# Performance work log

Hardware: AMD Instinct MI355X
Metric: run time of the kernel (lower is better)

## Reference

```python
import jax, jax.numpy as jnp
import numpy as np

NUM_HEADS = 16


def _local_attn(q, k, v, bias, nq, nk):
    """Blocked local attention, faithful to rearrange_to_dense_trunk semantics.
    q,k,v: [B,H,N,D]; bias: [B,Hb,N,N] (Hb broadcasts against H).
    Trunk i (queries [i*nq,(i+1)*nq)) attends keys at original indices
    [i*nq - pad_left, i*nq - pad_left + nk); out-of-range keys/values/bias are
    zero-padded (the module pads with zeros, no -inf key masking).
    Assumes N % nq == 0 (q_pad_length == 0, so the query mask loop is a no-op).
    """
    B, H, N, D = q.shape
    T = N // nq                      # n_trunks
    pad_left = (nk - nq) // 2
    Lp = (T - 1) * nq + nk           # padded key length so every window is full
    pad_right = Lp - pad_left - N
    k_p = jnp.pad(k, ((0, 0), (0, 0), (pad_left, pad_right), (0, 0)))
    v_p = jnp.pad(v, ((0, 0), (0, 0), (pad_left, pad_right), (0, 0)))
    b_p = jnp.pad(bias, ((0, 0), (0, 0), (0, 0), (pad_left, pad_right)))
    # window gather indices: [T, nk]
    kidx = jnp.arange(T)[:, None] * nq + jnp.arange(nk)[None, :]
    k_t = k_p[:, :, kidx, :]         # [B,H,T,nk,D]
    v_t = v_p[:, :, kidx, :]         # [B,H,T,nk,D]
    Bb, Hb = bias.shape[0], bias.shape[1]
    b_r = b_p.reshape(Bb, Hb, T, nq, Lp)
    b_t = jnp.take_along_axis(b_r, kidx[None, None, :, None, :], axis=-1)  # [Bb,Hb,T,nq,nk]
    q_t = q.reshape(B, H, T, nq, D)
    scores = jnp.einsum('bhtqd,bhtkd->bhtqk', q_t, k_t) + b_t
    w = jax.nn.softmax(scores, axis=-1)
    o = jnp.einsum('bhtqk,bhtkd->bhtqd', w, v_t)
    return o.reshape(B, H, N, D)


def setup_inputs() -> dict:
    key = jax.random.key(0)
    ks = jax.random.split(key, 8)
    B, N, C = 1, 4096, 256
    H, D = NUM_HEADS, 64
    HD = H * D
    q_x = jax.random.normal(ks[0], (B, N, C), dtype=jnp.float32)
    kv_x = jax.random.normal(ks[1], (B, N, C), dtype=jnp.float32)
    attn_bias = jax.random.normal(ks[2], (B, 1, N, N), dtype=jnp.float32) * 0.1
    Wq = jax.random.normal(ks[3], (C, HD), dtype=jnp.float32) / np.sqrt(C).astype(np.float32)
    Wk = jax.random.normal(ks[4], (C, HD), dtype=jnp.float32) / np.sqrt(C).astype(np.float32)
    Wv = jax.random.normal(ks[5], (C, HD), dtype=jnp.float32) / np.sqrt(C).astype(np.float32)
    Wg = jax.random.normal(ks[6], (C, HD), dtype=jnp.float32) / np.sqrt(C).astype(np.float32)
    Wo = jax.random.normal(ks[7], (HD, C), dtype=jnp.float32) / np.sqrt(HD).astype(np.float32)
    return {"q_x": q_x, "kv_x": kv_x, "attn_bias": attn_bias,
            "Wq": Wq, "Wk": Wk, "Wv": Wv, "Wg": Wg, "Wo": Wo,
            "n_queries": 64, "n_keys": 256}


def reference(q_x, kv_x, attn_bias, Wq, Wk, Wv, Wg, Wo, n_queries, n_keys):
    B, N, C = q_x.shape
    H = NUM_HEADS
    D = Wq.shape[-1] // H
    def split_heads(x):
        return x.reshape(B, N, H, D).transpose(0, 2, 1, 3)  # [B,H,N,D]
    q = split_heads(q_x @ Wq) / jnp.sqrt(jnp.float32(D))
    k = split_heads(kv_x @ Wk)
    v = split_heads(kv_x @ Wv)
    o = _local_attn(q, k, v, attn_bias, n_queries, n_keys)
    o = o.transpose(0, 2, 1, 3).reshape(B, N, H * D)
    g = jax.nn.sigmoid(q_x @ Wg)  # gating head
    return (o * g) @ Wo
```

## Files before the change

kernel.cpp:

```cpp
#include <hip/hip_runtime.h>

#define N_ 4096
#define C_ 256
#define H_ 16
#define D_ 64
#define HD_ 1024

typedef __attribute__((ext_vector_type(8))) _Float16 f16x8;
typedef __attribute__((ext_vector_type(4))) _Float16 f16x4;
typedef __attribute__((ext_vector_type(4))) float f32x4;

__device__ __forceinline__ void gload16(const void* g, void* l) {
    __builtin_amdgcn_global_load_lds(
        (const __attribute__((address_space(1))) unsigned int*)g,
        (__attribute__((address_space(3))) unsigned int*)l, 16, 0, 0);
}

__global__ __launch_bounds__(256) void convert_kernel(
    const float* __restrict__ q_x, const float* __restrict__ kv_x,
    const float* __restrict__ Wq, const float* __restrict__ Wk,
    const float* __restrict__ Wv, const float* __restrict__ Wg,
    const float* __restrict__ Wo,
    _Float16* __restrict__ Xf, _Float16* __restrict__ WTf,
    _Float16* __restrict__ WoTf)
{
    __shared__ float ts[64][65];
    const int b = blockIdx.x;
    const int tid = threadIdx.x;

    if (b < 512) {
        const int seg = b >> 8;
        const float* src = seg ? kv_x : q_x;
        _Float16* df = Xf + (size_t)seg * 1048576;
        const int base = (b & 255) * 4096 + tid * 16;
#pragma unroll
        for (int q = 0; q < 4; ++q) {
            float4 v = *(const float4*)&src[base + q * 4];
            f16x4 fv;
            fv[0] = (_Float16)v.x; fv[1] = (_Float16)v.y;
            fv[2] = (_Float16)v.z; fv[3] = (_Float16)v.w;
            *(f16x4*)&df[base + q * 4] = fv;
        }
        return;
    }

    const float* src;
    _Float16* df;
    int srcC, dstC, r0, c0;
    if (b < 768) {
        const int widx = (b - 512) >> 6;
        const int tile = (b - 512) & 63;
        src = (widx == 0) ? Wq : (widx == 1) ? Wk : (widx == 2) ? Wv : Wg;
        df = WTf + (size_t)widx * 262144;
        srcC = 1024; dstC = 256;
        r0 = (tile >> 4) * 64;
        c0 = (tile & 15) * 64;
    } else {
        const int tile = b - 768;
        src = Wo; df = WoTf;
        srcC = 256; dstC = 1024;
        r0 = (tile >> 2) * 64;
        c0 = (tile & 3) * 64;
    }
    {
        const int r = tid >> 2;
        const int cch = (tid & 3) * 16;
#pragma unroll
        for (int q = 0; q < 4; ++q) {
            float4 v = *(const float4*)&src[(size_t)(r0 + r) * srcC + c0 + cch + q * 4];
            ts[r][cch + q * 4 + 0] = v.x;
            ts[r][cch + q * 4 + 1] = v.y;
            ts[r][cch + q * 4 + 2] = v.z;
            ts[r][cch + q * 4 + 3] = v.w;
        }
    }
    __syncthreads();
    {
        const int c = tid >> 2;
        const int rch = (tid & 3) * 16;
#pragma unroll
        for (int q = 0; q < 4; ++q) {
            f16x4 fv;
#pragma unroll
            for (int j = 0; j < 4; ++j)
                fv[j] = (_Float16)ts[rch + q * 4 + j][c];
            *(f16x4*)&df[(size_t)(c0 + c) * dstC + r0 + rch + q * 4] = fv;
        }
    }
}

__global__ __launch_bounds__(256) void proj_mfma(
    const _Float16* __restrict__ Xf, const _Float16* __restrict__ WTf,
    _Float16* __restrict__ qh, _Float16* __restrict__ kh,
    _Float16* __restrict__ vt, _Float16* __restrict__ gh)
{
    __shared__ __align__(16) char psmem[24576];
    _Float16* As = (_Float16*)psmem;
    _Float16* Bs = (_Float16*)(psmem + 8192);

    const int lb  = blockIdx.x;
    const int xcd = lb & 7;
    const int gr  = (lb >> 6) * 8 + xcd;
    const int g   = gr >> 6;
    const int m0  = (gr & 63) * 64;
    const int c0  = ((lb >> 3) & 7) * 128;

    const _Float16* A = Xf + ((g == 1 || g == 2) ? 1048576 : 0);
    const _Float16* B = WTf + (size_t)g * 262144;

    const int tid  = threadIdx.x;
    const int wv   = tid >> 6;
    const int lane = tid & 63;
    const int frow = lane & 15;
    const int grp  = lane >> 4;

    f32x4 acc[8];
#pragma unroll
    for (int j = 0; j < 8; ++j) acc[j] = (f32x4){0.f, 0.f, 0.f, 0.f};

    const int srow = tid >> 3;
    const int sch  = tid & 7;

    for (int kt = 0; kt < 256; kt += 64) {
        __syncthreads();
#pragma unroll
        for (int p = 0; p < 2; ++p) {
            const int row = p * 32 + srow;
            const int koff = kt + ((sch ^ (row & 7)) << 3);
            gload16(A + (size_t)(m0 + row) * 256 + koff, (char*)As + p * 4096 + tid * 16);
        }
#pragma unroll
        for (int p = 0; p < 4; ++p) {
            const int row = p * 32 + srow;
            const int koff = kt + ((sch ^ (row & 7)) << 3);
            gload16(B + (size_t)(c0 + row) * 256 + koff, (char*)Bs + p * 4096 + tid * 16);
        }
        __syncthreads();

#pragma unroll
        for (int ks = 0; ks < 2; ++ks) {
            const int ra = wv * 16 + frow;
            const f16x8 af = *(const f16x8*)((char*)As + ra * 128 + (((ks * 4 + grp) ^ (ra & 7)) << 4));
#pragma unroll
            for (int j = 0; j < 8; ++j) {
                const int rb = j * 16 + frow;
                const f16x8 bf = *(const f16x8*)((char*)Bs + rb * 128 + (((ks * 4 + grp) ^ (rb & 7)) << 4));
                acc[j] = __builtin_amdgcn_mfma_f32_16x16x32_f16(af, bf, acc[j], 0, 0, 0);
            }
        }
    }

    if (g == 2) {
#pragma unroll
        for (int j = 0; j < 8; ++j) {
            const int dglob = c0 + j * 16 + frow;
            const int n = m0 + wv * 16 + grp * 4;
            f16x4 pv;
#pragma unroll
            for (int v = 0; v < 4; ++v) pv[v] = (_Float16)acc[j][v];
            *(f16x4*)&vt[((size_t)dglob << 12) + n] = pv;
        }
        return;
    }

    __syncthreads();
    _Float16* Epi = (_Float16*)psmem;
    {
        const float scale = (g == 0) ? 0.125f : 1.f;
#pragma unroll
        for (int j = 0; j < 8; ++j) {
            const int rr = wv * 16 + grp * 4;
            const int cc = j * 16 + frow;
#pragma unroll
            for (int v = 0; v < 4; ++v) {
                float x = acc[j][v];
                x = (g == 3) ? 1.f / (1.f + __expf(-x)) : x * scale;
                Epi[(rr + v) * 136 + cc] = (_Float16)x;
            }
        }
    }
    __syncthreads();
    {
        const int ch   = tid & 15;
        const int head = ch >> 3;
        const int e8   = (ch & 7) * 8;
#pragma unroll
        for (int p = 0; p < 4; ++p) {
            const int r = p * 16 + (tid >> 4);
            const f16x8 val = *(const f16x8*)&Epi[r * 136 + head * 64 + e8];
            const int n = m0 + r;
            if (g == 3) {
                *(f16x8*)&gh[(size_t)n * HD_ + c0 + head * 64 + e8] = val;
            } else {
                _Float16* dst = (g == 0) ? qh : kh;
                const int hh = (c0 >> 6) + head;
                *(f16x8*)&dst[((size_t)hh * N_ + n) * D_ + e8] = val;
            }
        }
    }
}

__global__ __launch_bounds__(256, 4) void attn_mfma(
    const _Float16* __restrict__ qh, const _Float16* __restrict__ kh,
    const _Float16* __restrict__ vt, const float* __restrict__ bias,
    const _Float16* __restrict__ gh, _Float16* __restrict__ of)
{
    __shared__ __align__(16) char smem[40960];
    _Float16* Qs = (_Float16*)smem;
    char* Ks = smem + 8192;
    char* Ps = smem;
    char* Vs = smem + 16384;
    float* Oe = (float*)smem;

    const int lb  = blockIdx.x;
    const int xcd = lb & 7;
    const int j_  = lb >> 3;
    const int h   = j_ >> 3;
    const int t   = xcd * 8 + (j_ & 7);
    const int tid = threadIdx.x;
    const int lane = tid & 63;
    const int wv = tid >> 6;
    const int frow = lane & 15;
    const int grp = lane >> 4;
    const int kbase = t * 64 - 96;

    const char* qbase = (const char*)qh + (size_t)(h * N_ + t * 64) * 128;
    const char* kbase_p = (const char*)kh + (size_t)h * N_ * 128;

#pragma unroll
    for (int q = 0; q < 2; ++q) {
        const int lin = q * 4096 + tid * 16;
        const int row = lin >> 7;
        const int ch = (lin >> 4) & 7;
        gload16(qbase + row * 128 + ((ch ^ (row & 7)) << 4), (char*)Qs + lin);
    }
#pragma unroll
    for (int q = 0; q < 8; ++q) {
        const int lin = q * 4096 + tid * 16;
        const int row = lin >> 7;
        const int ch = (lin >> 4) & 7;
        const int kg = kbase + row;
        if ((unsigned)kg < (unsigned)N_) {
            gload16(kbase_p + (size_t)kg * 128 + ((ch ^ (row & 7)) << 4), Ks + lin);
        } else {
            *(float4*)(Ks + lin) = make_float4(0.f, 0.f, 0.f, 0.f);
        }
    }

    f32x4 sacc[16];
    {
        const int rowg = t * 64 + wv * 16 + grp * 4;
#pragma unroll
        for (int j = 0; j < 16; ++j) {
            const int colg = kbase + j * 16 + frow;
            const bool ok = (unsigned)colg < (unsigned)N_;
#pragma unroll
            for (int v = 0; v < 4; ++v)
                sacc[j][v] = ok ? bias[(size_t)(rowg + v) * N_ + colg] : 0.f;
        }
    }
    __syncthreads();

    {
        const int rq = wv * 16 + frow;
#pragma unroll
        for (int ks = 0; ks < 2; ++ks) {
            const f16x8 aq = *(const f16x8*)((char*)Qs + rq * 128 + (((ks * 4 + grp) ^ (rq & 7)) << 4));
#pragma unroll
            for (int j = 0; j < 16; ++j) {
                const int rk = j * 16 + frow;
                const f16x8 bk = *(const f16x8*)(Ks + rk * 128 + (((ks * 4 + grp) ^ (rk & 7)) << 4));
                sacc[j] = __builtin_amdgcn_mfma_f32_16x16x32_f16(aq, bk, sacc[j], 0, 0, 0);
            }
        }
    }
    __syncthreads();

    float inv[4];
    f32x4 oacc[4];
#pragma unroll
    for (int jd = 0; jd < 4; ++jd) oacc[jd] = (f32x4){0.f, 0.f, 0.f, 0.f};

#pragma unroll
    for (int c = 0; c < 2; ++c) {
        const int cb = kbase + c * 128;
        const bool bnd = (c == 0) ? (t <= 1) : (t >= 62);
        {
#pragma unroll
            for (int q = 0; q < 4; ++q) {
                const int lin = q * 4096 + tid * 16;
                const int d  = lin >> 8;
                const int cs = (lin >> 4) & 15;
                const int cl = (cs & 8) | ((cs & 7) ^ (d & 7));
                const int kg0 = cb + cl * 8;
                const int kgc = kg0 < 0 ? 0 : (kg0 > N_ - 8 ? N_ - 8 : kg0);
                gload16(vt + (((size_t)(h * 64 + d)) << 12) + kgc, Vs + lin);
            }
        }
        if (c == 0) {
#pragma unroll
            for (int v = 0; v < 4; ++v) {
                float m = sacc[0][v];
#pragma unroll
                for (int f = 1; f < 16; ++f) m = fmaxf(m, sacc[f][v]);
                m = fmaxf(m, __shfl_xor(m, 1));
                m = fmaxf(m, __shfl_xor(m, 2));
                m = fmaxf(m, __shfl_xor(m, 4));
                m = fmaxf(m, __shfl_xor(m, 8));
                float l = 0.f;
#pragma unroll
                for (int f = 0; f < 16; ++f) {
                    float e = __expf(sacc[f][v] - m);
                    sacc[f][v] = e;
                    l += e;
                }
                l += __shfl_xor(l, 1);
                l += __shfl_xor(l, 2);
                l += __shfl_xor(l, 4);
                l += __shfl_xor(l, 8);
                inv[v] = 1.f / l;
            }
        }
        {
#pragma unroll
            for (int j = 0; j < 8; ++j) {
#pragma unroll
                for (int v = 0; v < 4; ++v) {
                    const int r = wv * 16 + grp * 4 + v;
                    const int byt = r * 256 + ((j * 32 + frow * 2) ^ ((r & 7) << 4));
                    *(_Float16*)(Ps + byt) = (_Float16)sacc[c * 8 + j][v];
                }
            }
        }
        __syncthreads();
        if (bnd) {
#pragma unroll
            for (int q = 0; q < 4; ++q) {
                const int lin = q * 4096 + tid * 16;
                const int d  = lin >> 8;
                const int cs = (lin >> 4) & 15;
                const int cl = (cs & 8) | ((cs & 7) ^ (d & 7));
                const int kg0 = cb + cl * 8;
                if ((unsigned)kg0 >= (unsigned)N_)
                    *(float4*)(Vs + lin) = make_float4(0.f, 0.f, 0.f, 0.f);
            }
            __syncthreads();
        }
        const int rp = wv * 16 + frow;
#pragma unroll
        for (int ks = 0; ks < 4; ++ks) {
            const f16x8 ap = *(const f16x8*)(Ps + rp * 256 + (((ks * 4 + grp) ^ (rp & 7)) << 4));
#pragma unroll
            for (int jd = 0; jd < 4; ++jd) {
                const int rd = jd * 16 + frow;
                const f16x8 bv = *(const f16x8*)(Vs + rd * 256 + (((ks * 4 + grp) ^ (rd & 7)) << 4));
                oacc[jd] = __builtin_amdgcn_mfma_f32_16x16x32_f16(ap, bv, oacc[jd], 0, 0, 0);
            }
        }
        __syncthreads();
    }

#pragma unroll
    for (int jd = 0; jd < 4; ++jd) {
        const int dcol = jd * 16 + frow;
#pragma unroll
        for (int v = 0; v < 4; ++v) {
            const int rn = wv * 16 + grp * 4 + v;
            Oe[rn * 68 + dcol] = oacc[jd][v] * inv[v];
        }
    }
    __syncthreads();
    {
        const int r   = tid >> 2;
        const int seg = tid & 3;
        const int n   = t * 64 + r;
        const int cg0 = h * 64 + seg * 16;
        const float* orow = &Oe[r * 68 + seg * 16];
        f32x4 o0 = *(const f32x4*)&orow[0];
        f32x4 o1 = *(const f32x4*)&orow[4];
        f32x4 o2 = *(const f32x4*)&orow[8];
        f32x4 o3 = *(const f32x4*)&orow[12];
        const f16x8 g0 = *(const f16x8*)&gh[(size_t)n * HD_ + cg0];
        const f16x8 g1 = *(const f16x8*)&gh[(size_t)n * HD_ + cg0 + 8];
        f16x8 r0, r1;
#pragma unroll
        for (int e = 0; e < 4; ++e) {
            r0[e]     = (_Float16)(o0[e] * (float)g0[e]);
            r0[4 + e] = (_Float16)(o1[e] * (float)g0[4 + e]);
            r1[e]     = (_Float16)(o2[e] * (float)g1[e]);
            r1[4 + e] = (_Float16)(o3[e] * (float)g1[4 + e]);
        }
        *(f16x8*)&of[(size_t)n * HD_ + cg0]     = r0;
        *(f16x8*)&of[(size_t)n * HD_ + cg0 + 8] = r1;
    }
}

__global__ __launch_bounds__(256) void out_mfma(
    const _Float16* __restrict__ of, const _Float16* __restrict__ WoTf,
    float* __restrict__ out)
{
    __shared__ __align__(16) char smem[24576];

    const int lb  = blockIdx.x;
    const int xcd = lb & 7;
    const int s   = lb >> 3;
    const int rowt = (s >> 2) * 8 + xcd;
    const int m0  = rowt * 32;
    const int c0  = (s & 3) * 64;

    const int tid  = threadIdx.x;
    const int wave = tid >> 6;
    const int lane = tid & 63;
    const int wr   = wave >> 1;
    const int wc   = wave & 1;
    const int frow = lane & 15;
    const int grp  = lane >> 4;

    f32x4 acc[2];
#pragma unroll
    for (int j = 0; j < 2; ++j) acc[j] = (f32x4){0.f, 0.f, 0.f, 0.f};

    auto STAGE = [&](char* bb, int kt) {
        {
            const int row = tid >> 3;
            const int ch  = tid & 7;
            const int koff = kt + ((ch ^ (row & 7)) << 3);
            gload16(of + (size_t)(m0 + row) * HD_ + koff, bb + tid * 16);
        }
#pragma unroll
        for (int p = 0; p < 2; ++p) {
            const int lin = p * 4096 + tid * 16;
            const int row = lin >> 7;
            const int ch  = (lin >> 4) & 7;
            const int koff = kt + ((ch ^ (row & 7)) << 3);
            gload16(WoTf + (size_t)(c0 + row) * HD_ + koff, bb + 4096 + lin);
        }
    };

    STAGE(smem, 0);
    __syncthreads();

    for (int t = 0; t < 16; ++t) {
        char* cur = smem + (t & 1) * 12288;
        if (t < 15) STAGE(smem + ((t + 1) & 1) * 12288, (t + 1) * 64);

        _Float16* As = (_Float16*)cur;
        _Float16* Bs = (_Float16*)(cur + 4096);
#pragma unroll
        for (int ks = 0; ks < 2; ++ks) {
            const int ra = wr * 16 + frow;
            const f16x8 af = *(const f16x8*)((char*)As + ra * 128 + (((ks * 4 + grp) ^ (ra & 7)) << 4));
#pragma unroll
            for (int j = 0; j < 2; ++j) {
                const int rb = wc * 32 + j * 16 + frow;
                const f16x8 bf = *(const f16x8*)((char*)Bs + rb * 128 + (((ks * 4 + grp) ^ (rb & 7)) << 4));
                acc[j] = __builtin_amdgcn_mfma_f32_16x16x32_f16(af, bf, acc[j], 0, 0, 0);
            }
        }
        __syncthreads();
    }

    const int rbase = grp * 4;
#pragma unroll
    for (int j = 0; j < 2; ++j) {
        const int c = c0 + wc * 32 + j * 16 + frow;
#pragma unroll
        for (int v = 0; v < 4; ++v) {
            const int n = m0 + wr * 16 + rbase + v;
            out[(size_t)n * C_ + c] = acc[j][v];
        }
    }
}

extern "C" void kernel_launch(void* const* d_in, const int* in_sizes, int n_in,
                              void* d_out, int out_size, void* d_ws, size_t ws_size,
                              hipStream_t stream)
{
    const float* q_x  = (const float*)d_in[0];
    const float* kv_x = (const float*)d_in[1];
    const float* bias = (const float*)d_in[2];
    const float* Wq   = (const float*)d_in[3];
    const float* Wk   = (const float*)d_in[4];
    const float* Wv   = (const float*)d_in[5];
    const float* Wg   = (const float*)d_in[6];
    const float* Wo   = (const float*)d_in[7];
    float* out = (float*)d_out;

    char* ws = (char*)d_ws;
    const size_t MB = 1048576;
    _Float16* qh   = (_Float16*)(ws);
    _Float16* kh   = (_Float16*)(ws + 8  * MB);
    _Float16* vt   = (_Float16*)(ws + 16 * MB);
    _Float16* gh   = (_Float16*)(ws + 24 * MB);
    _Float16* of   = (_Float16*)(ws + 32 * MB);
    _Float16* Xf   = (_Float16*)(ws + 40 * MB);
    _Float16* WTf  = (_Float16*)(ws + 44 * MB);
    _Float16* WoTf = (_Float16*)(ws + 46 * MB);

    convert_kernel<<<832, 256, 0, stream>>>(q_x, kv_x, Wq, Wk, Wv, Wg, Wo,
                                            Xf, WTf, WoTf);
    proj_mfma<<<2048, 256, 0, stream>>>(Xf, WTf, qh, kh, vt, gh);
    attn_mfma<<<1024, 256, 0, stream>>>(qh, kh, vt, bias, gh, of);
    out_mfma<<<512, 256, 0, stream>>>(of, WoTf, out);
}
```

Before: 161.5 us.

## Pre-pack bias windows transposed for vector loads; shrink out-projection tiles

```diff
diff --git a/kernel.cpp b/kernel.cpp
--- a/kernel.cpp
+++ b/kernel.cpp
@@ -18,11 +18,12 @@
 
 __global__ __launch_bounds__(256) void convert_kernel(
     const float* __restrict__ q_x, const float* __restrict__ kv_x,
+    const float* __restrict__ bias,
     const float* __restrict__ Wq, const float* __restrict__ Wk,
     const float* __restrict__ Wv, const float* __restrict__ Wg,
     const float* __restrict__ Wo,
     _Float16* __restrict__ Xf, _Float16* __restrict__ WTf,
-    _Float16* __restrict__ WoTf)
+    _Float16* __restrict__ WoTf, float* __restrict__ bpF)
 {
     __shared__ float ts[64][65];
     const int b = blockIdx.x;
@@ -40,6 +41,45 @@
             fv[0] = (_Float16)v.x; fv[1] = (_Float16)v.y;
             fv[2] = (_Float16)v.z; fv[3] = (_Float16)v.w;
             *(f16x4*)&df[base + q * 4] = fv;
+        }
+        return;
+    }
+
+    if (b >= 832) {
+        const int t = b - 832;
+        const int kb = t * 64 - 96;
+        float* bpT = bpF + (size_t)t * 16384;
+#pragma unroll
+        for (int cc = 0; cc < 4; ++cc) {
+            if (cc) __syncthreads();
+            {
+                const int q = tid >> 2;
+                const float* brow = bias + (size_t)(t * 64 + q) * 4096;
+#pragma unroll
+                for (int u = 0; u < 4; ++u) {
+                    const int lc = (tid & 3) * 16 + u * 4;
+                    const int kg = kb + cc * 64 + lc;
+                    float4 v = make_float4(0.f, 0.f, 0.f, 0.f);
+                    if ((unsigned)kg < 4093u) v = *(const float4*)&brow[kg];
+                    ts[q][lc + 0] = v.x; ts[q][lc + 1] = v.y;
+                    ts[q][lc + 2] = v.z; ts[q][lc + 3] = v.w;
+                }
+            }
+            __syncthreads();
+            {
+                const int s = tid >> 2;
+                const int qseg = (tid & 3) * 16;
+                float* drow = bpT + (size_t)(cc * 64 + s) * 64 + qseg;
+#pragma unroll
+                for (int u = 0; u < 4; ++u) {
+                    float4 v;
+                    v.x = ts[qseg + u * 4 + 0][s];
+                    v.y = ts[qseg + u * 4 + 1][s];
+                    v.z = ts[qseg + u * 4 + 2][s];
+                    v.w = ts[qseg + u * 4 + 3][s];
+                    *(float4*)&drow[u * 4] = v;
+                }
+            }
         }
         return;
     }
@@ -202,7 +242,7 @@
 
 __global__ __launch_bounds__(256, 4) void attn_mfma(
     const _Float16* __restrict__ qh, const _Float16* __restrict__ kh,
-    const _Float16* __restrict__ vt, const float* __restrict__ bias,
+    const _Float16* __restrict__ vt, const float* __restrict__ bpF,
     const _Float16* __restrict__ gh, _Float16* __restrict__ of)
 {
     __shared__ __align__(16) char smem[40960];
@@ -249,15 +289,11 @@
 
     f32x4 sacc[16];
     {
-        const int rowg = t * 64 + wv * 16 + grp * 4;
-#pragma unroll
-        for (int j = 0; j < 16; ++j) {
-            const int colg = kbase + j * 16 + frow;
-            const bool ok = (unsigned)colg < (unsigned)N_;
-#pragma unroll
-            for (int v = 0; v < 4; ++v)
-                sacc[j][v] = ok ? bias[(size_t)(rowg + v) * N_ + colg] : 0.f;
-        }
+        const float* bpT = bpF + (size_t)t * 16384;
+        const int q0 = wv * 16 + grp * 4;
+#pragma unroll
+        for (int j = 0; j < 16; ++j)
+            sacc[j] = *(const f32x4*)&bpT[(j * 16 + frow) * 64 + q0];
     }
     __syncthreads();
 
@@ -399,14 +435,14 @@
     const _Float16* __restrict__ of, const _Float16* __restrict__ WoTf,
     float* __restrict__ out)
 {
-    __shared__ __align__(16) char smem[24576];
+    __shared__ __align__(16) char smem[16384];
 
     const int lb  = blockIdx.x;
     const int xcd = lb & 7;
     const int s   = lb >> 3;
-    const int rowt = (s >> 2) * 8 + xcd;
+    const int rowt = (s >> 3) * 8 + xcd;
     const int m0  = rowt * 32;
-    const int c0  = (s & 3) * 64;
+    const int c0  = (s & 7) * 32;
 
     const int tid  = threadIdx.x;
     const int wave = tid >> 6;
@@ -416,33 +452,22 @@
     const int frow = lane & 15;
     const int grp  = lane >> 4;
 
-    f32x4 acc[2];
-#pragma unroll
-    for (int j = 0; j < 2; ++j) acc[j] = (f32x4){0.f, 0.f, 0.f, 0.f};
+    f32x4 acc = (f32x4){0.f, 0.f, 0.f, 0.f};
 
     auto STAGE = [&](char* bb, int kt) {
-        {
-            const int row = tid >> 3;
-            const int ch  = tid & 7;
-            const int koff = kt + ((ch ^ (row & 7)) << 3);
-            gload16(of + (size_t)(m0 + row) * HD_ + koff, bb + tid * 16);
-        }
-#pragma unroll
-        for (int p = 0; p < 2; ++p) {
-            const int lin = p * 4096 + tid * 16;
-            const int row = lin >> 7;
-            const int ch  = (lin >> 4) & 7;
-            const int koff = kt + ((ch ^ (row & 7)) << 3);
-            gload16(WoTf + (size_t)(c0 + row) * HD_ + koff, bb + 4096 + lin);
-        }
+        const int row = tid >> 3;
+        const int ch  = tid & 7;
+        const int koff = kt + ((ch ^ (row & 7)) << 3);
+        gload16(of + (size_t)(m0 + row) * HD_ + koff, bb + tid * 16);
+        gload16(WoTf + (size_t)(c0 + row) * HD_ + koff, bb + 4096 + tid * 16);
     };
 
     STAGE(smem, 0);
     __syncthreads();
 
     for (int t = 0; t < 16; ++t) {
-        char* cur = smem + (t & 1) * 12288;
-        if (t < 15) STAGE(smem + ((t + 1) & 1) * 12288, (t + 1) * 64);
+        char* cur = smem + (t & 1) * 8192;
+        if (t < 15) STAGE(smem + ((t + 1) & 1) * 8192, (t + 1) * 64);
 
         _Float16* As = (_Float16*)cur;
         _Float16* Bs = (_Float16*)(cur + 4096);
@@ -450,24 +475,20 @@
         for (int ks = 0; ks < 2; ++ks) {
             const int ra = wr * 16 + frow;
             const f16x8 af = *(const f16x8*)((char*)As + ra * 128 + (((ks * 4 + grp) ^ (ra & 7)) << 4));
-#pragma unroll
-            for (int j = 0; j < 2; ++j) {
-                const int rb = wc * 32 + j * 16 + frow;
-                const f16x8 bf = *(const f16x8*)((char*)Bs + rb * 128 + (((ks * 4 + grp) ^ (rb & 7)) << 4));
-                acc[j] = __builtin_amdgcn_mfma_f32_16x16x32_f16(af, bf, acc[j], 0, 0, 0);
-            }
+            const int rb = wc * 16 + frow;
+            const f16x8 bf = *(const f16x8*)((char*)Bs + rb * 128 + (((ks * 4 + grp) ^ (rb & 7)) << 4));
+            acc = __builtin_amdgcn_mfma_f32_16x16x32_f16(af, bf, acc, 0, 0, 0);
         }
         __syncthreads();
     }
 
-    const int rbase = grp * 4;
-#pragma unroll
-    for (int j = 0; j < 2; ++j) {
-        const int c = c0 + wc * 32 + j * 16 + frow;
+    {
+        const int c = c0 + wc * 16 + frow;
+        const int rbase = grp * 4;
 #pragma unroll
         for (int v = 0; v < 4; ++v) {
             const int n = m0 + wr * 16 + rbase + v;
-            out[(size_t)n * C_ + c] = acc[j][v];
+            out[(size_t)n * C_ + c] = acc[v];
         }
     }
 }
@@ -496,10 +517,11 @@
     _Float16* Xf   = (_Float16*)(ws + 40 * MB);
     _Float16* WTf  = (_Float16*)(ws + 44 * MB);
     _Float16* WoTf = (_Float16*)(ws + 46 * MB);
-
-    convert_kernel<<<832, 256, 0, stream>>>(q_x, kv_x, Wq, Wk, Wv, Wg, Wo,
-                                            Xf, WTf, WoTf);
+    float*    bpF  = (float*)   (ws + 48 * MB);
+
+    convert_kernel<<<896, 256, 0, stream>>>(q_x, kv_x, bias, Wq, Wk, Wv, Wg, Wo,
+                                            Xf, WTf, WoTf, bpF);
     proj_mfma<<<2048, 256, 0, stream>>>(Xf, WTf, qh, kh, vt, gh);
-    attn_mfma<<<1024, 256, 0, stream>>>(qh, kh, vt, bias, gh, of);
-    out_mfma<<<512, 256, 0, stream>>>(of, WoTf, out);
+    attn_mfma<<<1024, 256, 0, stream>>>(qh, kh, vt, bpF, gh, of);
+    out_mfma<<<1024, 256, 0, stream>>>(of, WoTf, out);
 }
```

New measurement: 161.6 us. No clear change (+0.0%).

## Fuse all four stages into one persistent cooperative kernel with grid syncs

Applied to the files above, without the earlier changes.

```diff
diff --git a/kernel.cpp b/kernel.cpp
--- a/kernel.cpp
+++ b/kernel.cpp
@@ -1,4 +1,7 @@
 #include <hip/hip_runtime.h>
+#include <hip/hip_cooperative_groups.h>
+
+namespace cg = cooperative_groups;
 
 #define N_ 4096
 #define C_ 256
@@ -14,6 +17,462 @@
     __builtin_amdgcn_global_load_lds(
         (const __attribute__((address_space(1))) unsigned int*)g,
         (__attribute__((address_space(3))) unsigned int*)l, 16, 0, 0);
+}
+
+__device__ __forceinline__ void phase_sync(cg::grid_group& g) {
+    __threadfence();
+    g.sync();
+    __threadfence();
+}
+
+__global__ __launch_bounds__(256) void fused_all(
+    const float* __restrict__ q_x, const float* __restrict__ kv_x,
+    const float* __restrict__ bias,
+    const float* __restrict__ Wq, const float* __restrict__ Wk,
+    const float* __restrict__ Wv, const float* __restrict__ Wg,
+    const float* __restrict__ Wo,
+    _Float16* __restrict__ Xf, _Float16* __restrict__ WTf,
+    _Float16* __restrict__ WoTf,
+    _Float16* __restrict__ qh, _Float16* __restrict__ kh,
+    _Float16* __restrict__ vt, _Float16* __restrict__ gh,
+    _Float16* __restrict__ of, float* __restrict__ out)
+{
+    __shared__ __align__(16) char smem[40960];
+    cg::grid_group grid = cg::this_grid();
+    const int nb  = gridDim.x;
+    const int bid = blockIdx.x;
+    const int tid = threadIdx.x;
+
+    for (int b = bid; b < 832; b += nb) {
+        float (*ts)[65] = (float(*)[65])smem;
+        if (b < 512) {
+            const int seg = b >> 8;
+            const float* src = seg ? kv_x : q_x;
+            _Float16* df = Xf + (size_t)seg * 1048576;
+            const int base = (b & 255) * 4096 + tid * 16;
+#pragma unroll
+            for (int q = 0; q < 4; ++q) {
+                float4 v = *(const float4*)&src[base + q * 4];
+                f16x4 fv;
+                fv[0] = (_Float16)v.x; fv[1] = (_Float16)v.y;
+                fv[2] = (_Float16)v.z; fv[3] = (_Float16)v.w;
+                *(f16x4*)&df[base + q * 4] = fv;
+            }
+        } else {
+            const float* src;
+            _Float16* df;
+            int srcC, dstC, r0, c0;
+            if (b < 768) {
+                const int widx = (b - 512) >> 6;
+                const int tile = (b - 512) & 63;
+                src = (widx == 0) ? Wq : (widx == 1) ? Wk : (widx == 2) ? Wv : Wg;
+                df = WTf + (size_t)widx * 262144;
+                srcC = 1024; dstC = 256;
+                r0 = (tile >> 4) * 64;
+                c0 = (tile & 15) * 64;
+            } else {
+                const int tile = b - 768;
+                src = Wo; df = WoTf;
+                srcC = 256; dstC = 1024;
+                r0 = (tile >> 2) * 64;
+                c0 = (tile & 3) * 64;
+            }
+            {
+                const int r = tid >> 2;
+                const int cch = (tid & 3) * 16;
+#pragma unroll
+                for (int q = 0; q < 4; ++q) {
+                    float4 v = *(const float4*)&src[(size_t)(r0 + r) * srcC + c0 + cch + q * 4];
+                    ts[r][cch + q * 4 + 0] = v.x;
+                    ts[r][cch + q * 4 + 1] = v.y;
+                    ts[r][cch + q * 4 + 2] = v.z;
+                    ts[r][cch + q * 4 + 3] = v.w;
+                }
+            }
+            __syncthreads();
+            {
+                const int c = tid >> 2;
+                const int rch = (tid & 3) * 16;
+#pragma unroll
+                for (int q = 0; q < 4; ++q) {
+                    f16x4 fv;
+#pragma unroll
+                    for (int j = 0; j < 4; ++j)
+                        fv[j] = (_Float16)ts[rch + q * 4 + j][c];
+                    *(f16x4*)&df[(size_t)(c0 + c) * dstC + r0 + rch + q * 4] = fv;
+                }
+            }
+            __syncthreads();
+        }
+    }
+    phase_sync(grid);
+
+    for (int lb = bid; lb < 2048; lb += nb) {
+        _Float16* As = (_Float16*)smem;
+        _Float16* Bs = (_Float16*)(smem + 8192);
+
+        const int xcd = lb & 7;
+        const int gr  = (lb >> 6) * 8 + xcd;
+        const int g   = gr >> 6;
+        const int m0  = (gr & 63) * 64;
+        const int c0  = ((lb >> 3) & 7) * 128;
+
+        const _Float16* A = Xf + ((g == 1 || g == 2) ? 1048576 : 0);
+        const _Float16* B = WTf + (size_t)g * 262144;
+
+        const int wv   = tid >> 6;
+        const int lane = tid & 63;
+        const int frow = lane & 15;
+        const int grp  = lane >> 4;
+
+        f32x4 acc[8];
+#pragma unroll
+        for (int j = 0; j < 8; ++j) acc[j] = (f32x4){0.f, 0.f, 0.f, 0.f};
+
+        const int srow = tid >> 3;
+        const int sch  = tid & 7;
+
+        for (int kt = 0; kt < 256; kt += 64) {
+            __syncthreads();
+#pragma unroll
+            for (int p = 0; p < 2; ++p) {
+                const int row = p * 32 + srow;
+                const int koff = kt + ((sch ^ (row & 7)) << 3);
+                gload16(A + (size_t)(m0 + row) * 256 + koff, (char*)As + p * 4096 + tid * 16);
+            }
+#pragma unroll
+            for (int p = 0; p < 4; ++p) {
+                const int row = p * 32 + srow;
+                const int koff = kt + ((sch ^ (row & 7)) << 3);
+                gload16(B + (size_t)(c0 + row) * 256 + koff, (char*)Bs + p * 4096 + tid * 16);
+            }
+            __syncthreads();
+
+#pragma unroll
+            for (int ks = 0; ks < 2; ++ks) {
+                const int ra = wv * 16 + frow;
+                const f16x8 af = *(const f16x8*)((char*)As + ra * 128 + (((ks * 4 + grp) ^ (ra & 7)) << 4));
+#pragma unroll
+                for (int j = 0; j < 8; ++j) {
+                    const int rb = j * 16 + frow;
+                    const f16x8 bf = *(const f16x8*)((char*)Bs + rb * 128 + (((ks * 4 + grp) ^ (rb & 7)) << 4));
+                    acc[j] = __builtin_amdgcn_mfma_f32_16x16x32_f16(af, bf, acc[j], 0, 0, 0);
+                }
+            }
+        }
+
+        if (g == 2) {
+#pragma unroll
+            for (int j = 0; j < 8; ++j) {
+                const int dglob = c0 + j * 16 + frow;
+                const int n = m0 + wv * 16 + grp * 4;
+                f16x4 pv;
+#pragma unroll
+                for (int v = 0; v < 4; ++v) pv[v] = (_Float16)acc[j][v];
+                *(f16x4*)&vt[((size_t)dglob << 12) + n] = pv;
+            }
+            __syncthreads();
+        } else {
+            __syncthreads();
+            _Float16* Epi = (_Float16*)smem;
+            {
+                const float scale = (g == 0) ? 0.125f : 1.f;
+#pragma unroll
+                for (int j = 0; j < 8; ++j) {
+                    const int rr = wv * 16 + grp * 4;
+                    const int cc = j * 16 + frow;
+#pragma unroll
+                    for (int v = 0; v < 4; ++v) {
+                        float x = acc[j][v];
+                        x = (g == 3) ? 1.f / (1.f + __expf(-x)) : x * scale;
+                        Epi[(rr + v) * 136 + cc] = (_Float16)x;
+                    }
+                }
+            }
+            __syncthreads();
+            {
+                const int ch   = tid & 15;
+                const int head = ch >> 3;
+                const int e8   = (ch & 7) * 8;
+#pragma unroll
+                for (int p = 0; p < 4; ++p) {
+                    const int r = p * 16 + (tid >> 4);
+                    const f16x8 val = *(const f16x8*)&Epi[r * 136 + head * 64 + e8];
+                    const int n = m0 + r;
+                    if (g == 3) {
+                        *(f16x8*)&gh[(size_t)n * HD_ + c0 + head * 64 + e8] = val;
+                    } else {
+                        _Float16* dst = (g == 0) ? qh : kh;
+                        const int hh = (c0 >> 6) + head;
+                        *(f16x8*)&dst[((size_t)hh * N_ + n) * D_ + e8] = val;
+                    }
+                }
+            }
+            __syncthreads();
+        }
+    }
+    phase_sync(grid);
+
+    for (int ab = bid; ab < 1024; ab += nb) {
+        _Float16* Qs = (_Float16*)smem;
+        char* Ks = smem + 8192;
+        char* Ps = smem;
+        char* Vs = smem + 16384;
+        float* Oe = (float*)smem;
+
+        const int xcd = ab & 7;
+        const int j_  = ab >> 3;
+        const int h   = j_ >> 3;
+        const int t   = xcd * 8 + (j_ & 7);
+        const int lane = tid & 63;
+        const int wv = tid >> 6;
+        const int frow = lane & 15;
+        const int grp = lane >> 4;
+        const int kbase = t * 64 - 96;
+
+        const char* qbase = (const char*)qh + (size_t)(h * N_ + t * 64) * 128;
+        const char* kbase_p = (const char*)kh + (size_t)h * N_ * 128;
+
+#pragma unroll
+        for (int q = 0; q < 2; ++q) {
+            const int lin = q * 4096 + tid * 16;
+            const int row = lin >> 7;
+            const int ch = (lin >> 4) & 7;
+            gload16(qbase + row * 128 + ((ch ^ (row & 7)) << 4), (char*)Qs + lin);
+        }
+#pragma unroll
+        for (int q = 0; q < 8; ++q) {
+            const int lin = q * 4096 + tid * 16;
+            const int row = lin >> 7;
+            const int ch = (lin >> 4) & 7;
+            const int kg = kbase + row;
+            if ((unsigned)kg < (unsigned)N_) {
+                gload16(kbase_p + (size_t)kg * 128 + ((ch ^ (row & 7)) << 4), Ks + lin);
+            } else {
+                *(float4*)(Ks + lin) = make_float4(0.f, 0.f, 0.f, 0.f);
+            }
+        }
+
+        f32x4 sacc[16];
+        {
+            const int rowg = t * 64 + wv * 16 + grp * 4;
+#pragma unroll
+            for (int j = 0; j < 16; ++j) {
+                const int colg = kbase + j * 16 + frow;
+                const bool ok = (unsigned)colg < (unsigned)N_;
+#pragma unroll
+                for (int v = 0; v < 4; ++v)
+                    sacc[j][v] = ok ? bias[(size_t)(rowg + v) * N_ + colg] : 0.f;
+            }
+        }
+        __syncthreads();
+
+        {
+            const int rq = wv * 16 + frow;
+#pragma unroll
+            for (int ks = 0; ks < 2; ++ks) {
+                const f16x8 aq = *(const f16x8*)((char*)Qs + rq * 128 + (((ks * 4 + grp) ^ (rq & 7)) << 4));
+#pragma unroll
+                for (int j = 0; j < 16; ++j) {
+                    const int rk = j * 16 + frow;
+                    const f16x8 bk = *(const f16x8*)(Ks + rk * 128 + (((ks * 4 + grp) ^ (rk & 7)) << 4));
+                    sacc[j] = __builtin_amdgcn_mfma_f32_16x16x32_f16(aq, bk, sacc[j], 0, 0, 0);
+                }
+            }
+        }
+        __syncthreads();
+
+        float inv[4];
+        f32x4 oacc[4];
+#pragma unroll
+        for (int jd = 0; jd < 4; ++jd) oacc[jd] = (f32x4){0.f, 0.f, 0.f, 0.f};
+
+#pragma unroll
+        for (int c = 0; c < 2; ++c) {
+            const int cb = kbase + c * 128;
+            const bool bnd = (c == 0) ? (t <= 1) : (t >= 62);
+            {
+#pragma unroll
+                for (int q = 0; q < 4; ++q) {
+                    const int lin = q * 4096 + tid * 16;
+                    const int d  = lin >> 8;
+                    const int cs = (lin >> 4) & 15;
+                    const int cl = (cs & 8) | ((cs & 7) ^ (d & 7));
+                    const int kg0 = cb + cl * 8;
+                    const int kgc = kg0 < 0 ? 0 : (kg0 > N_ - 8 ? N_ - 8 : kg0);
+                    gload16(vt + (((size_t)(h * 64 + d)) << 12) + kgc, Vs + lin);
+                }
+            }
+            if (c == 0) {
+#pragma unroll
+                for (int v = 0; v < 4; ++v) {
+                    float m = sacc[0][v];
+#pragma unroll
+                    for (int f = 1; f < 16; ++f) m = fmaxf(m, sacc[f][v]);
+                    m = fmaxf(m, __shfl_xor(m, 1));
+                    m = fmaxf(m, __shfl_xor(m, 2));
+                    m = fmaxf(m, __shfl_xor(m, 4));
+                    m = fmaxf(m, __shfl_xor(m, 8));
+                    float l = 0.f;
+#pragma unroll
+                    for (int f = 0; f < 16; ++f) {
+                        float e = __expf(sacc[f][v] - m);
+                        sacc[f][v] = e;
+                        l += e;
+                    }
+                    l += __shfl_xor(l, 1);
+                    l += __shfl_xor(l, 2);
+                    l += __shfl_xor(l, 4);
+                    l += __shfl_xor(l, 8);
+                    inv[v] = 1.f / l;
+                }
+            }
+            {
+#pragma unroll
+                for (int j = 0; j < 8; ++j) {
+#pragma unroll
+                    for (int v = 0; v < 4; ++v) {
+                        const int r = wv * 16 + grp * 4 + v;
+                        const int byt = r * 256 + ((j * 32 + frow * 2) ^ ((r & 7) << 4));
+                        *(_Float16*)(Ps + byt) = (_Float16)sacc[c * 8 + j][v];
+                    }
+                }
+            }
+            __syncthreads();
+            if (bnd) {
+#pragma unroll
+                for (int q = 0; q < 4; ++q) {
+                    const int lin = q * 4096 + tid * 16;
+                    const int d  = lin >> 8;
+                    const int cs = (lin >> 4) & 15;
+                    const int cl = (cs & 8) | ((cs & 7) ^ (d & 7));
+                    const int kg0 = cb + cl * 8;
+                    if ((unsigned)kg0 >= (unsigned)N_)
+                        *(float4*)(Vs + lin) = make_float4(0.f, 0.f, 0.f, 0.f);
+                }
+                __syncthreads();
+            }
+            const int rp = wv * 16 + frow;
+#pragma unroll
+            for (int ks = 0; ks < 4; ++ks) {
+                const f16x8 ap = *(const f16x8*)(Ps + rp * 256 + (((ks * 4 + grp) ^ (rp & 7)) << 4));
+#pragma unroll
+                for (int jd = 0; jd < 4; ++jd) {
+                    const int rd = jd * 16 + frow;
+                    const f16x8 bv = *(const f16x8*)(Vs + rd * 256 + (((ks * 4 + grp) ^ (rd & 7)) << 4));
+                    oacc[jd] = __builtin_amdgcn_mfma_f32_16x16x32_f16(ap, bv, oacc[jd], 0, 0, 0);
+                }
+            }
+            __syncthreads();
+        }
+
+#pragma unroll
+        for (int jd = 0; jd < 4; ++jd) {
+            const int dcol = jd * 16 + frow;
+#pragma unroll
+            for (int v = 0; v < 4; ++v) {
+                const int rn = wv * 16 + grp * 4 + v;
+                Oe[rn * 68 + dcol] = oacc[jd][v] * inv[v];
+            }
+        }
+        __syncthreads();
+        {
+            const int r   = tid >> 2;
+            const int seg = tid & 3;
+            const int n   = t * 64 + r;
+            const int cg0 = h * 64 + seg * 16;
+            const float* orow = &Oe[r * 68 + seg * 16];
+            f32x4 o0 = *(const f32x4*)&orow[0];
+            f32x4 o1 = *(const f32x4*)&orow[4];
+            f32x4 o2 = *(const f32x4*)&orow[8];
+            f32x4 o3 = *(const f32x4*)&orow[12];
+            const f16x8 g0 = *(const f16x8*)&gh[(size_t)n * HD_ + cg0];
+            const f16x8 g1 = *(const f16x8*)&gh[(size_t)n * HD_ + cg0 + 8];
+            f16x8 r0, r1;
+#pragma unroll
+            for (int e = 0; e < 4; ++e) {
+                r0[e]     = (_Float16)(o0[e] * (float)g0[e]);
+                r0[4 + e] = (_Float16)(o1[e] * (float)g0[4 + e]);
+                r1[e]     = (_Float16)(o2[e] * (float)g1[e]);
+                r1[4 + e] = (_Float16)(o3[e] * (float)g1[4 + e]);
+            }
+            *(f16x8*)&of[(size_t)n * HD_ + cg0]     = r0;
+            *(f16x8*)&of[(size_t)n * HD_ + cg0 + 8] = r1;
+        }
+        __syncthreads();
+    }
+    phase_sync(grid);
+
+    for (int ob = bid; ob < 512; ob += nb) {
+        const int xcd = ob & 7;
+        const int s   = ob >> 3;
+        const int rowt = (s >> 2) * 8 + xcd;
+        const int m0  = rowt * 32;
+        const int c0  = (s & 3) * 64;
+
+        const int wave = tid >> 6;
+        const int lane = tid & 63;
+        const int wr   = wave >> 1;
+        const int wc   = wave & 1;
+        const int frow = lane & 15;
+        const int grp  = lane >> 4;
+
+        f32x4 acc[2];
+#pragma unroll
+        for (int j = 0; j < 2; ++j) acc[j] = (f32x4){0.f, 0.f, 0.f, 0.f};
+
+        auto STAGE = [&](char* bb, int kt) {
+            {
+                const int row = tid >> 3;
+                const int ch  = tid & 7;
+                const int koff = kt + ((ch ^ (row & 7)) << 3);
+                gload16(of + (size_t)(m0 + row) * HD_ + koff, bb + tid * 16);
+            }
+#pragma unroll
+            for (int p = 0; p < 2; ++p) {
+                const int lin = p * 4096 + tid * 16;
+                const int row = lin >> 7;
+                const int ch  = (lin >> 4) & 7;
+                const int koff = kt + ((ch ^ (row & 7)) << 3);
+                gload16(WoTf + (size_t)(c0 + row) * HD_ + koff, bb + 4096 + lin);
+            }
+        };
+
+        __syncthreads();
+        STAGE(smem, 0);
+        __syncthreads();
+
+        for (int t = 0; t < 16; ++t) {
+            char* cur = smem + (t & 1) * 12288;
+            if (t < 15) STAGE(smem + ((t + 1) & 1) * 12288, (t + 1) * 64);
+
+            _Float16* As = (_Float16*)cur;
+            _Float16* Bs = (_Float16*)(cur + 4096);
+#pragma unroll
+            for (int ks = 0; ks < 2; ++ks) {
+                const int ra = wr * 16 + frow;
+                const f16x8 af = *(const f16x8*)((char*)As + ra * 128 + (((ks * 4 + grp) ^ (ra & 7)) << 4));
+#pragma unroll
+                for (int j = 0; j < 2; ++j) {
+                    const int rb = wc * 32 + j * 16 + frow;
+                    const f16x8 bf = *(const f16x8*)((char*)Bs + rb * 128 + (((ks * 4 + grp) ^ (rb & 7)) << 4));
+                    acc[j] = __builtin_amdgcn_mfma_f32_16x16x32_f16(af, bf, acc[j], 0, 0, 0);
+                }
+            }
+            __syncthreads();
+        }
+
+        const int rbase = grp * 4;
+#pragma unroll
+        for (int j = 0; j < 2; ++j) {
+            const int c = c0 + wc * 32 + j * 16 + frow;
+#pragma unroll
+            for (int v = 0; v < 4; ++v) {
+                const int n = m0 + wr * 16 + rbase + v;
+                out[(size_t)n * C_ + c] = acc[j][v];
+            }
+        }
+    }
 }
 
 __global__ __launch_bounds__(256) void convert_kernel(
@@ -497,6 +956,25 @@
     _Float16* WTf  = (_Float16*)(ws + 44 * MB);
     _Float16* WoTf = (_Float16*)(ws + 46 * MB);
 
+    int occ = 0;
+    hipError_t qe = hipOccupancyMaxActiveBlocksPerMultiprocessor(
+        &occ, (const void*)fused_all, 256, 0);
+    int nb = (qe == hipSuccess && occ > 0) ? occ * 256 : 0;
+    if (nb > 1024) nb = 1024;
+
+    if (nb >= 8) {
+        void* args[] = {
+            (void*)&q_x, (void*)&kv_x, (void*)&bias,
+            (void*)&Wq, (void*)&Wk, (void*)&Wv, (void*)&Wg, (void*)&Wo,
+            (void*)&Xf, (void*)&WTf, (void*)&WoTf,
+            (void*)&qh, (void*)&kh, (void*)&vt, (void*)&gh,
+            (void*)&of, (void*)&out
+        };
+        if (hipLaunchCooperativeKernel((const void*)fused_all, dim3(nb),
+                                       dim3(256), args, 0, stream) == hipSuccess)
+            return;
+    }
+
     convert_kernel<<<832, 256, 0, stream>>>(q_x, kv_x, Wq, Wk, Wv, Wg, Wo,
                                             Xf, WTf, WoTf);
     proj_mfma<<<2048, 256, 0, stream>>>(Xf, WTf, qh, kh, vt, gh);
```

Result: no change. 161.9 us (+0.2%).

## Pre-pack banded attention bias into transposed fp16 tiles once per trunk

Applied to the files above, without the earlier changes.

```diff
diff --git a/kernel.cpp b/kernel.cpp
--- a/kernel.cpp
+++ b/kernel.cpp
@@ -18,11 +18,12 @@
 
 __global__ __launch_bounds__(256) void convert_kernel(
     const float* __restrict__ q_x, const float* __restrict__ kv_x,
+    const float* __restrict__ bias,
     const float* __restrict__ Wq, const float* __restrict__ Wk,
     const float* __restrict__ Wv, const float* __restrict__ Wg,
     const float* __restrict__ Wo,
     _Float16* __restrict__ Xf, _Float16* __restrict__ WTf,
-    _Float16* __restrict__ WoTf)
+    _Float16* __restrict__ WoTf, _Float16* __restrict__ bpH)
 {
     __shared__ float ts[64][65];
     const int b = blockIdx.x;
@@ -40,6 +41,45 @@
             fv[0] = (_Float16)v.x; fv[1] = (_Float16)v.y;
             fv[2] = (_Float16)v.z; fv[3] = (_Float16)v.w;
             *(f16x4*)&df[base + q * 4] = fv;
+        }
+        return;
+    }
+
+    if (b >= 832) {
+        const int t = b - 832;
+        const int kb = t * 64 - 96;
+        _Float16* bpT = bpH + (size_t)t * 16384;
+#pragma unroll
+        for (int cc = 0; cc < 4; ++cc) {
+            if (cc) __syncthreads();
+            {
+                const int q = tid >> 2;
+                const float* brow = bias + (size_t)(t * 64 + q) * 4096;
+#pragma unroll
+                for (int u = 0; u < 4; ++u) {
+                    const int lc = (tid & 3) * 16 + u * 4;
+                    const int kg = kb + cc * 64 + lc;
+                    float4 v = make_float4(0.f, 0.f, 0.f, 0.f);
+                    if ((unsigned)kg < 4093u) v = *(const float4*)&brow[kg];
+                    ts[q][lc + 0] = v.x; ts[q][lc + 1] = v.y;
+                    ts[q][lc + 2] = v.z; ts[q][lc + 3] = v.w;
+                }
+            }
+            __syncthreads();
+            {
+                const int s = tid >> 2;
+                const int qseg = (tid & 3) * 16;
+                _Float16* drow = bpT + (size_t)(cc * 64 + s) * 64 + qseg;
+#pragma unroll
+                for (int u = 0; u < 4; ++u) {
+                    f16x4 v;
+                    v[0] = (_Float16)ts[qseg + u * 4 + 0][s];
+                    v[1] = (_Float16)ts[qseg + u * 4 + 1][s];
+                    v[2] = (_Float16)ts[qseg + u * 4 + 2][s];
+                    v[3] = (_Float16)ts[qseg + u * 4 + 3][s];
+                    *(f16x4*)&drow[u * 4] = v;
+                }
+            }
         }
         return;
     }
@@ -202,7 +242,7 @@
 
 __global__ __launch_bounds__(256, 4) void attn_mfma(
     const _Float16* __restrict__ qh, const _Float16* __restrict__ kh,
-    const _Float16* __restrict__ vt, const float* __restrict__ bias,
+    const _Float16* __restrict__ vt, const _Float16* __restrict__ bpH,
     const _Float16* __restrict__ gh, _Float16* __restrict__ of)
 {
     __shared__ __align__(16) char smem[40960];
@@ -249,14 +289,13 @@
 
     f32x4 sacc[16];
     {
-        const int rowg = t * 64 + wv * 16 + grp * 4;
+        const _Float16* bpT = bpH + (size_t)t * 16384;
+        const int q0 = wv * 16 + grp * 4;
 #pragma unroll
         for (int j = 0; j < 16; ++j) {
-            const int colg = kbase + j * 16 + frow;
-            const bool ok = (unsigned)colg < (unsigned)N_;
-#pragma unroll
-            for (int v = 0; v < 4; ++v)
-                sacc[j][v] = ok ? bias[(size_t)(rowg + v) * N_ + colg] : 0.f;
+            const f16x4 bv = *(const f16x4*)&bpT[(j * 16 + frow) * 64 + q0];
+#pragma unroll
+            for (int v = 0; v < 4; ++v) sacc[j][v] = (float)bv[v];
         }
     }
     __syncthreads();
@@ -496,10 +535,11 @@
     _Float16* Xf   = (_Float16*)(ws + 40 * MB);
     _Float16* WTf  = (_Float16*)(ws + 44 * MB);
     _Float16* WoTf = (_Float16*)(ws + 46 * MB);
-
-    convert_kernel<<<832, 256, 0, stream>>>(q_x, kv_x, Wq, Wk, Wv, Wg, Wo,
-                                            Xf, WTf, WoTf);
+    _Float16* bpH  = (_Float16*)(ws + 48 * MB);
+
+    convert_kernel<<<896, 256, 0, stream>>>(q_x, kv_x, bias, Wq, Wk, Wv, Wg, Wo,
+                                            Xf, WTf, WoTf, bpH);
     proj_mfma<<<2048, 256, 0, stream>>>(Xf, WTf, qh, kh, vt, gh);
-    attn_mfma<<<1024, 256, 0, stream>>>(qh, kh, vt, bias, gh, of);
+    attn_mfma<<<1024, 256, 0, stream>>>(qh, kh, vt, bpH, gh, of);
     out_mfma<<<512, 256, 0, stream>>>(of, WoTf, out);
 }
```

Measured after the change: 165.5 us. 1.02x slower.
